# Kernel optimization log

Measured on AMD Instinct MI355X. Metric: run time of the kernel, lower is better.

## Reference

```python
import jax, jax.numpy as jnp
import numpy as np

N_NODES = 100000
N_EDGES = 1200000
D_IN = 64
D_HID = 64


def _sage_conv(x, src, dst, W_l, W_r, b, num_nodes):
    # PyG SAGEConv (mean aggr): out = mean_{j in N(i)} x_j @ W_l^T + x_i @ W_r^T + b
    msgs = x[src]                                                   # [E, d] gather
    summed = jax.ops.segment_sum(msgs, dst, num_segments=num_nodes)  # [N, d] scatter-add
    cnt = jax.ops.segment_sum(jnp.ones((src.shape[0],), x.dtype), dst,
                              num_segments=num_nodes)                # [N]
    agg = summed / jnp.maximum(cnt, 1.0)[:, None]                    # mean, safe for isolated nodes
    return agg @ W_l.T + x @ W_r.T + b


def setup_inputs() -> dict:
    key = jax.random.key(0)
    ks = jax.random.split(key, 8)
    x = jax.random.normal(ks[0], (N_NODES, D_IN), dtype=jnp.float32)
    edge_index = jax.random.randint(ks[1], (2, N_EDGES), 0, N_NODES, dtype=jnp.int32)
    s = 1.0 / np.sqrt(D_IN)
    W1_l = jax.random.uniform(ks[2], (D_HID, D_IN), jnp.float32, -s, s)
    W1_r = jax.random.uniform(ks[3], (D_HID, D_IN), jnp.float32, -s, s)
    b1 = jnp.zeros((D_HID,), jnp.float32)
    s2 = 1.0 / np.sqrt(D_HID)
    W2_l = jax.random.uniform(ks[4], (D_HID, D_HID), jnp.float32, -s2, s2)
    W2_r = jax.random.uniform(ks[5], (D_HID, D_HID), jnp.float32, -s2, s2)
    b2 = jnp.zeros((D_HID,), jnp.float32)
    return {"x": x, "edge_index": edge_index, "W1_l": W1_l, "W1_r": W1_r, "b1": b1,
            "W2_l": W2_l, "W2_r": W2_r, "b2": b2}


def reference(x, edge_index, W1_l, W1_r, b1, W2_l, W2_r, b2):
    src, dst = edge_index[0], edge_index[1]  # messages flow src -> dst
    n = x.shape[0]
    h = _sage_conv(x, src, dst, W1_l, W1_r, b1, n)
    h = jax.nn.relu(h)  # dropout is identity in eval mode
    h = _sage_conv(h, src, dst, W2_l, W2_r, b2, n)
    return h
```

## Files before the change

kernel.cpp:

```cpp
#include <hip/hip_runtime.h>
#include <hip/hip_fp16.h>

#define NN 100000
#define NE 1200000
#define D 64
#define TBM 64
#define NBK 391
#define BSH 8
#define BMSK 255
#define CAP 4096
#define BINB 768

__global__ __launch_bounds__(256) void k_prep_bin(
    const float* __restrict__ in, __half* __restrict__ outh, int n8,
    const int* __restrict__ src, const int* __restrict__ dst,
    int* __restrict__ cur, int* __restrict__ eidx, int E) {
  int tid = threadIdx.x;
  if (blockIdx.x < BINB) {
    __shared__ int lhist[NBK];
    __shared__ int lbase[NBK];
    int chunk = (E + BINB - 1) / BINB;
    int e0 = blockIdx.x * chunk;
    int e1 = min(e0 + chunk, E);

    for (int i = tid; i < NBK; i += 256) lhist[i] = 0;
    __syncthreads();
    for (int e = e0 + tid; e < e1; e += 256) atomicAdd(&lhist[dst[e] >> BSH], 1);
    __syncthreads();
    for (int i = tid; i < NBK; i += 256) {
      int c = lhist[i];
      lbase[i] = c ? atomicAdd(&cur[i], c) : 0;
    }
    __syncthreads();
    for (int i = tid; i < NBK; i += 256) lhist[i] = 0;
    __syncthreads();
    for (int e = e0 + tid; e < e1; e += 256) {
      int d = dst[e];
      int b = d >> BSH;
      int r = atomicAdd(&lhist[b], 1);
      int p = lbase[b] + r;
      if (p < CAP) eidx[b * CAP + p] = ((d & BMSK) << 20) | src[e];
    }
  } else {
    int i = (blockIdx.x - BINB) * 256 + tid;
    if (i >= n8) return;
    float4 a = ((const float4*)in)[2 * i];
    float4 b = ((const float4*)in)[2 * i + 1];
    union { __half2 h; unsigned u; } p0, p1, p2, p3;
    p0.h = __floats2half2_rn(a.x, a.y);
    p1.h = __floats2half2_rn(a.z, a.w);
    p2.h = __floats2half2_rn(b.x, b.y);
    p3.h = __floats2half2_rn(b.z, b.w);
    uint4 o = {p0.u, p1.u, p2.u, p3.u};
    ((uint4*)outh)[i] = o;
  }
}

__global__ __launch_bounds__(256) void k_sort(int* __restrict__ eidx,
                                              const int* __restrict__ cur,
                                              int* __restrict__ off,
                                              int* __restrict__ deg, int N) {
  __shared__ int recS[CAP];
  __shared__ int srtS[CAP];
  __shared__ int hist[256];
  __shared__ int scan[256];
  __shared__ int cursor[256];

  int b = blockIdx.x;
  int tid = threadIdx.x;
  int cnt = min(cur[b], CAP);
  int ebase = b * CAP;

  for (int i = tid; i < cnt; i += 256) recS[i] = eidx[ebase + i];
  hist[tid] = 0;
  __syncthreads();
  for (int i = tid; i < cnt; i += 256) atomicAdd(&hist[recS[i] >> 20], 1);
  __syncthreads();

  int v = hist[tid];
  scan[tid] = v;
  __syncthreads();
  for (int o = 1; o < 256; o <<= 1) {
    int add = (tid >= o) ? scan[tid - o] : 0;
    __syncthreads();
    scan[tid] += add;
    __syncthreads();
  }
  int excl = scan[tid] - v;
  cursor[tid] = excl;
  __syncthreads();

  for (int i = tid; i < cnt; i += 256) {
    int rec = recS[i];
    int p = atomicAdd(&cursor[rec >> 20], 1);
    srtS[p] = rec & 0xFFFFF;
  }
  __syncthreads();
  for (int i = tid; i < cnt; i += 256) eidx[ebase + i] = srtS[i];

  int node = (b << BSH) + tid;
  if (node < N) {
    off[node] = ebase + excl;
    deg[node] = v;
  }
}

template <int RELU, int OUTH>
__global__ __launch_bounds__(256, 4) void sage_layer(
    const __half* __restrict__ feat,
    const int* __restrict__ off,
    const int* __restrict__ deg,
    const int* __restrict__ eidx,
    const float* __restrict__ Wl,
    const float* __restrict__ Wr,
    const float* __restrict__ bias,
    void* __restrict__ outp,
    int N) {
  __shared__ __align__(16) float At[TBM * 68];
  __shared__ __align__(16) float Wt[64 * 68];

  int tid = threadIdx.x;
  int tx = tid & 15;
  int ty = tid >> 4;
  int base = blockIdx.x * TBM;

  {
    int g = tid >> 2;
    int lane = tid & 3;
    int node = base + g;
    __half2 h0 = __float2half2_rn(0.f), h1 = h0, h2 = h0, h3 = h0;
    __half2 h4 = h0, h5 = h0, h6 = h0, h7 = h0;
    float inv = 1.0f;
    if (node < N) {
      int start = off[node];
      int cnt = deg[node];
      const uint4* f4 = (const uint4*)feat;
      union { unsigned x; __half2 h; } c;
      int j = 0;
#define ACC8(U0, U1)                                                   \
      c.x = U0.x; h0 = __hadd2(h0, c.h);                               \
      c.x = U0.y; h1 = __hadd2(h1, c.h);                               \
      c.x = U0.z; h2 = __hadd2(h2, c.h);                               \
      c.x = U0.w; h3 = __hadd2(h3, c.h);                               \
      c.x = U1.x; h4 = __hadd2(h4, c.h);                               \
      c.x = U1.y; h5 = __hadd2(h5, c.h);                               \
      c.x = U1.z; h6 = __hadd2(h6, c.h);                               \
      c.x = U1.w; h7 = __hadd2(h7, c.h);
      for (; j + 4 <= cnt; j += 4) {
        int s0 = eidx[start + j];
        int s1 = eidx[start + j + 1];
        int s2 = eidx[start + j + 2];
        int s3 = eidx[start + j + 3];
        uint4 u0 = f4[(size_t)s0 * 8 + lane * 2];
        uint4 u1 = f4[(size_t)s0 * 8 + lane * 2 + 1];
        uint4 v0 = f4[(size_t)s1 * 8 + lane * 2];
        uint4 v1 = f4[(size_t)s1 * 8 + lane * 2 + 1];
        uint4 w0 = f4[(size_t)s2 * 8 + lane * 2];
        uint4 w1 = f4[(size_t)s2 * 8 + lane * 2 + 1];
        uint4 x0 = f4[(size_t)s3 * 8 + lane * 2];
        uint4 x1 = f4[(size_t)s3 * 8 + lane * 2 + 1];
        ACC8(u0, u1)
        ACC8(v0, v1)
        ACC8(w0, w1)
        ACC8(x0, x1)
      }
      for (; j < cnt; ++j) {
        int s0 = eidx[start + j];
        uint4 u0 = f4[(size_t)s0 * 8 + lane * 2];
        uint4 u1 = f4[(size_t)s0 * 8 + lane * 2 + 1];
        ACC8(u0, u1)
      }
#undef ACC8
      inv = 1.0f / fmaxf((float)cnt, 1.0f);
    }
    float2 t0 = __half22float2(h0), t1 = __half22float2(h1);
    float2 t2 = __half22float2(h2), t3 = __half22float2(h3);
    float2 t4 = __half22float2(h4), t5 = __half22float2(h5);
    float2 t6 = __half22float2(h6), t7 = __half22float2(h7);
    float* dst = At + g * 68 + lane * 16;
    *(float4*)(dst + 0)  = make_float4(t0.x * inv, t0.y * inv, t1.x * inv, t1.y * inv);
    *(float4*)(dst + 4)  = make_float4(t2.x * inv, t2.y * inv, t3.x * inv, t3.y * inv);
    *(float4*)(dst + 8)  = make_float4(t4.x * inv, t4.y * inv, t5.x * inv, t5.y * inv);
    *(float4*)(dst + 12) = make_float4(t6.x * inv, t6.y * inv, t7.x * inv, t7.y * inv);
  }
#pragma unroll 1
  for (int i = 0; i < 4; ++i) {
    int f = tid + 256 * i;
    int k = f & 63;
    int n4 = f >> 6;
    float4 w;
    w.x = Wl[(4 * n4 + 0) * D + k];
    w.y = Wl[(4 * n4 + 1) * D + k];
    w.z = Wl[(4 * n4 + 2) * D + k];
    w.w = Wl[(4 * n4 + 3) * D + k];
    *(float4*)(Wt + k * 68 + 4 * n4) = w;
  }
  __syncthreads();

  float acc[4][4];
#pragma unroll
  for (int i = 0; i < 4; ++i)
#pragma unroll
    for (int j = 0; j < 4; ++j) acc[i][j] = 0.f;

#pragma unroll 2
  for (int kq = 0; kq < 16; ++kq) {
    float4 a0 = *(const float4*)(At + (4 * ty + 0) * 68 + 4 * kq);
    float4 a1 = *(const float4*)(At + (4 * ty + 1) * 68 + 4 * kq);
    float4 a2 = *(const float4*)(At + (4 * ty + 2) * 68 + 4 * kq);
    float4 a3 = *(const float4*)(At + (4 * ty + 3) * 68 + 4 * kq);
    float4 w0 = *(const float4*)(Wt + (4 * kq + 0) * 68 + 4 * tx);
    float4 w1 = *(const float4*)(Wt + (4 * kq + 1) * 68 + 4 * tx);
    float4 w2 = *(const float4*)(Wt + (4 * kq + 2) * 68 + 4 * tx);
    float4 w3 = *(const float4*)(Wt + (4 * kq + 3) * 68 + 4 * tx);
#define ROW(i, a)                                                      \
    acc[i][0] += a.x * w0.x; acc[i][1] += a.x * w0.y;                  \
    acc[i][2] += a.x * w0.z; acc[i][3] += a.x * w0.w;                  \
    acc[i][0] += a.y * w1.x; acc[i][1] += a.y * w1.y;                  \
    acc[i][2] += a.y * w1.z; acc[i][3] += a.y * w1.w;                  \
    acc[i][0] += a.z * w2.x; acc[i][1] += a.z * w2.y;                  \
    acc[i][2] += a.z * w2.z; acc[i][3] += a.z * w2.w;                  \
    acc[i][0] += a.w * w3.x; acc[i][1] += a.w * w3.y;                  \
    acc[i][2] += a.w * w3.z; acc[i][3] += a.w * w3.w;
    ROW(0, a0) ROW(1, a1) ROW(2, a2) ROW(3, a3)
  }
  __syncthreads();

#pragma unroll 1
  for (int i = 0; i < 4; ++i) {
    int f = tid + 256 * i;
    int row = f >> 4;
    int c4 = f & 15;
    int node = base + row;
    float4 v = make_float4(0.f, 0.f, 0.f, 0.f);
    if (node < N) {
      uint2 u = ((const uint2*)feat)[(size_t)node * 16 + c4];
      union { unsigned x; __half2 h; } c;
      c.x = u.x; float2 f0 = __half22float2(c.h);
      c.x = u.y; float2 f1 = __half22float2(c.h);
      v = make_float4(f0.x, f0.y, f1.x, f1.y);
    }
    *(float4*)(At + row * 68 + 4 * c4) = v;
  }
#pragma unroll 1
  for (int i = 0; i < 4; ++i) {
    int f = tid + 256 * i;
    int k = f & 63;
    int n4 = f >> 6;
    float4 w;
    w.x = Wr[(4 * n4 + 0) * D + k];
    w.y = Wr[(4 * n4 + 1) * D + k];
    w.z = Wr[(4 * n4 + 2) * D + k];
    w.w = Wr[(4 * n4 + 3) * D + k];
    *(float4*)(Wt + k * 68 + 4 * n4) = w;
  }
  __syncthreads();

#pragma unroll 2
  for (int kq = 0; kq < 16; ++kq) {
    float4 a0 = *(const float4*)(At + (4 * ty + 0) * 68 + 4 * kq);
    float4 a1 = *(const float4*)(At + (4 * ty + 1) * 68 + 4 * kq);
    float4 a2 = *(const float4*)(At + (4 * ty + 2) * 68 + 4 * kq);
    float4 a3 = *(const float4*)(At + (4 * ty + 3) * 68 + 4 * kq);
    float4 w0 = *(const float4*)(Wt + (4 * kq + 0) * 68 + 4 * tx);
    float4 w1 = *(const float4*)(Wt + (4 * kq + 1) * 68 + 4 * tx);
    float4 w2 = *(const float4*)(Wt + (4 * kq + 2) * 68 + 4 * tx);
    float4 w3 = *(const float4*)(Wt + (4 * kq + 3) * 68 + 4 * tx);
    ROW(0, a0) ROW(1, a1) ROW(2, a2) ROW(3, a3)
#undef ROW
  }

  float4 bv = ((const float4*)bias)[tx];
#pragma unroll
  for (int i = 0; i < 4; ++i) {
    int node = base + 4 * ty + i;
    if (node < N) {
      float4 o;
      o.x = acc[i][0] + bv.x;
      o.y = acc[i][1] + bv.y;
      o.z = acc[i][2] + bv.z;
      o.w = acc[i][3] + bv.w;
      if (RELU) {
        o.x = fmaxf(o.x, 0.f); o.y = fmaxf(o.y, 0.f);
        o.z = fmaxf(o.z, 0.f); o.w = fmaxf(o.w, 0.f);
      }
      if (OUTH) {
        union { __half2 h; unsigned u; } p0, p1;
        p0.h = __floats2half2_rn(o.x, o.y);
        p1.h = __floats2half2_rn(o.z, o.w);
        uint2 ov = {p0.u, p1.u};
        ((uint2*)outp)[(size_t)node * 16 + tx] = ov;
      } else {
        ((float4*)outp)[(size_t)node * 16 + tx] = o;
      }
    }
  }
}

extern "C" void kernel_launch(void* const* d_in, const int* in_sizes, int n_in,
                              void* d_out, int out_size, void* d_ws, size_t ws_size,
                              hipStream_t stream) {
  const float* x   = (const float*)d_in[0];
  const int* edge  = (const int*)d_in[1];
  const float* W1l = (const float*)d_in[2];
  const float* W1r = (const float*)d_in[3];
  const float* b1  = (const float*)d_in[4];
  const float* W2l = (const float*)d_in[5];
  const float* W2r = (const float*)d_in[6];
  const float* b2  = (const float*)d_in[7];
  float* out = (float*)d_out;

  const int N = NN, E = NE;
  const int* src = edge;
  const int* dst = edge + E;

  int* cur    = (int*)d_ws;
  int* eidx   = cur + 512;
  int* off    = eidx + (size_t)NBK * CAP;
  int* deg    = off + N;
  __half* x_h = (__half*)(deg + N);
  __half* h_h = x_h + (size_t)N * D;

  const int n8 = N * D / 8;
  const int gridT = (N + TBM - 1) / TBM;
  const int gridPB = BINB + (n8 + 255) / 256;

  hipMemsetAsync(cur, 0, 512 * sizeof(int), stream);
  k_prep_bin<<<gridPB, 256, 0, stream>>>(x, x_h, n8, src, dst, cur, eidx, E);
  k_sort<<<NBK, 256, 0, stream>>>(eidx, cur, off, deg, N);

  sage_layer<1, 1><<<gridT, 256, 0, stream>>>(x_h, off, deg, eidx,
                                              W1l, W1r, b1, h_h, N);
  sage_layer<0, 0><<<gridT, 256, 0, stream>>>(h_h, off, deg, eidx,
                                              W2l, W2r, b2, out, N);
}
```

Baseline: 137.3 us.

## Split prep and binning kernels, fold memset, sort neighbor lists by source

The fused prep/bin kernel is split into a fp16 conversion kernel that also zeroes the bin counters, replacing the hipMemsetAsync, and a separate binning kernel. In k_sort each thread insertion-sorts its node's neighbor list by source index, so the later gathers touch feature rows in ascending order for better cache locality. This adds one kernel launch and a serial per-thread sort of about 12 elements in shared memory, and it removes the memset launch and the overlap between conversion and binning.

```diff
diff --git a/kernel.cpp b/kernel.cpp
--- a/kernel.cpp
+++ b/kernel.cpp
@@ -9,50 +9,52 @@
 #define BSH 8
 #define BMSK 255
 #define CAP 4096
-#define BINB 768
-
-__global__ __launch_bounds__(256) void k_prep_bin(
-    const float* __restrict__ in, __half* __restrict__ outh, int n8,
-    const int* __restrict__ src, const int* __restrict__ dst,
-    int* __restrict__ cur, int* __restrict__ eidx, int E) {
+
+__global__ __launch_bounds__(256) void k_prep(const float* __restrict__ in,
+                                              __half* __restrict__ outh, int n8,
+                                              int* __restrict__ cur) {
+  int i = blockIdx.x * 256 + threadIdx.x;
+  if (i < 512) cur[i] = 0;
+  if (i >= n8) return;
+  float4 a = ((const float4*)in)[2 * i];
+  float4 b = ((const float4*)in)[2 * i + 1];
+  union { __half2 h; unsigned u; } p0, p1, p2, p3;
+  p0.h = __floats2half2_rn(a.x, a.y);
+  p1.h = __floats2half2_rn(a.z, a.w);
+  p2.h = __floats2half2_rn(b.x, b.y);
+  p3.h = __floats2half2_rn(b.z, b.w);
+  uint4 o = {p0.u, p1.u, p2.u, p3.u};
+  ((uint4*)outh)[i] = o;
+}
+
+__global__ __launch_bounds__(256) void k_bin(const int* __restrict__ src,
+                                             const int* __restrict__ dst,
+                                             int* __restrict__ cur,
+                                             int* __restrict__ eidx, int E) {
+  __shared__ int lhist[NBK];
+  __shared__ int lbase[NBK];
   int tid = threadIdx.x;
-  if (blockIdx.x < BINB) {
-    __shared__ int lhist[NBK];
-    __shared__ int lbase[NBK];
-    int chunk = (E + BINB - 1) / BINB;
-    int e0 = blockIdx.x * chunk;
-    int e1 = min(e0 + chunk, E);
-
-    for (int i = tid; i < NBK; i += 256) lhist[i] = 0;
-    __syncthreads();
-    for (int e = e0 + tid; e < e1; e += 256) atomicAdd(&lhist[dst[e] >> BSH], 1);
-    __syncthreads();
-    for (int i = tid; i < NBK; i += 256) {
-      int c = lhist[i];
-      lbase[i] = c ? atomicAdd(&cur[i], c) : 0;
-    }
-    __syncthreads();
-    for (int i = tid; i < NBK; i += 256) lhist[i] = 0;
-    __syncthreads();
-    for (int e = e0 + tid; e < e1; e += 256) {
-      int d = dst[e];
-      int b = d >> BSH;
-      int r = atomicAdd(&lhist[b], 1);
-      int p = lbase[b] + r;
-      if (p < CAP) eidx[b * CAP + p] = ((d & BMSK) << 20) | src[e];
-    }
-  } else {
-    int i = (blockIdx.x - BINB) * 256 + tid;
-    if (i >= n8) return;
-    float4 a = ((const float4*)in)[2 * i];
-    float4 b = ((const float4*)in)[2 * i + 1];
-    union { __half2 h; unsigned u; } p0, p1, p2, p3;
-    p0.h = __floats2half2_rn(a.x, a.y);
-    p1.h = __floats2half2_rn(a.z, a.w);
-    p2.h = __floats2half2_rn(b.x, b.y);
-    p3.h = __floats2half2_rn(b.z, b.w);
-    uint4 o = {p0.u, p1.u, p2.u, p3.u};
-    ((uint4*)outh)[i] = o;
+  int chunk = (E + gridDim.x - 1) / gridDim.x;
+  int e0 = blockIdx.x * chunk;
+  int e1 = min(e0 + chunk, E);
+
+  for (int i = tid; i < NBK; i += 256) lhist[i] = 0;
+  __syncthreads();
+  for (int e = e0 + tid; e < e1; e += 256) atomicAdd(&lhist[dst[e] >> BSH], 1);
+  __syncthreads();
+  for (int i = tid; i < NBK; i += 256) {
+    int c = lhist[i];
+    lbase[i] = c ? atomicAdd(&cur[i], c) : 0;
+  }
+  __syncthreads();
+  for (int i = tid; i < NBK; i += 256) lhist[i] = 0;
+  __syncthreads();
+  for (int e = e0 + tid; e < e1; e += 256) {
+    int d = dst[e];
+    int b = d >> BSH;
+    int r = atomicAdd(&lhist[b], 1);
+    int p = lbase[b] + r;
+    if (p < CAP) eidx[b * CAP + p] = ((d & BMSK) << 20) | src[e];
   }
 }
 
@@ -96,6 +98,18 @@
     srtS[p] = rec & 0xFFFFF;
   }
   __syncthreads();
+
+  {
+    int s0 = excl, s1 = excl + v;
+    for (int i = s0 + 1; i < s1; ++i) {
+      int key = srtS[i];
+      int j = i - 1;
+      while (j >= s0 && srtS[j] > key) { srtS[j + 1] = srtS[j]; --j; }
+      srtS[j + 1] = key;
+    }
+  }
+  __syncthreads();
+
   for (int i = tid; i < cnt; i += 256) eidx[ebase + i] = srtS[i];
 
   int node = (b << BSH) + tid;
@@ -321,12 +335,11 @@
   __half* x_h = (__half*)(deg + N);
   __half* h_h = x_h + (size_t)N * D;
 
-  const int n8 = N * D / 8;
   const int gridT = (N + TBM - 1) / TBM;
-  const int gridPB = BINB + (n8 + 255) / 256;
-
-  hipMemsetAsync(cur, 0, 512 * sizeof(int), stream);
-  k_prep_bin<<<gridPB, 256, 0, stream>>>(x, x_h, n8, src, dst, cur, eidx, E);
+  const int gridC = (N * D / 8 + 255) / 256;
+
+  k_prep<<<gridC, 256, 0, stream>>>(x, x_h, N * D / 8, cur);
+  k_bin<<<768, 256, 0, stream>>>(src, dst, cur, eidx, E);
   k_sort<<<NBK, 256, 0, stream>>>(eidx, cur, off, deg, N);
 
   sage_layer<1, 1><<<gridT, 256, 0, stream>>>(x_h, off, deg, eidx,
```

Measured after the change: 164.6 us. 19.9% more time.
